# Kernel tuning notes

Measured on AMD Instinct MI355X. Metric: run time of the kernel, lower is better.

The kernel has to match this reference:

```python
import jax, jax.numpy as jnp
import numpy as np

GROUP_SIZE = 128
EQN = "btd,kdf->btkf"  # x:[B,T,D] @ w:[K,D,F] -> [B,T,K,F]


def setup_inputs() -> dict:
    key = jax.random.key(0)
    k1, k2, k3, k4 = jax.random.split(key, 4)
    B, T, D = 4, 2048, 4096
    K, F = 2, 8192
    G = D // GROUP_SIZE  # 32 quantization groups along D
    x = jax.random.normal(k1, (B, T, D), dtype=jnp.float32)
    qweight = jax.random.randint(k2, (K, D, F), 0, 16, dtype=jnp.int32)  # uint4 values
    qzeros = jax.random.randint(k3, (K, G, F), 0, 16, dtype=jnp.int32)   # uint4 zero points
    scales = jax.random.uniform(k4, (K, G, F), dtype=jnp.float32) * 0.02
    return {"x": x, "qweight": qweight, "qzeros": qzeros, "scales": scales}


def dequantize(imatrix, scales, zeros, group_size, axis_to_repeat):
    rs = jnp.repeat(scales, group_size, axis=axis_to_repeat)
    rz = jnp.repeat(zeros, group_size, axis=axis_to_repeat)
    return (imatrix.astype(rs.dtype) - rz.astype(rs.dtype)) * rs


def reference(x, qweight, qzeros, scales):
    # dequantize int4 weights along axis 1 (hidden/contraction dim), then einsum
    w = dequantize(qweight, scales, qzeros, GROUP_SIZE, axis_to_repeat=1)  # [K,D,F] fp32
    w = w.astype(x.dtype)
    return jnp.einsum(EQN, x, w)  # [B,T,K,F]
```

## Files before the change

kernel.cpp:

```cpp
#include <hip/hip_runtime.h>
#include <hip/hip_bf16.h>
#include <stdint.h>


typedef __attribute__((ext_vector_type(8))) short bf16x8;
typedef __attribute__((ext_vector_type(16))) float f32x16;
typedef __attribute__((ext_vector_type(4))) float f32x4;

static constexpr int Dd = 4096, Ff = 8192;
static constexpr int M = 8192, NTOT = 16384;
static constexpr int NKT = Dd / 64;
static constexpr int NMB = M / 256;
static constexpr int NNB = NTOT / 256;

__device__ __forceinline__ short f2bf(float f) {
    __hip_bfloat16 h = __float2bfloat16(f);
    return *reinterpret_cast<short*>(&h);
}

__device__ __forceinline__ int frag_off(int r, int cb) {
    const int rb = r >> 5, ks = cb >> 1, kh = cb & 1;
    return ((rb * 4 + ks) << 10) + (((r & 31) + 32 * kh) << 4);
}

__global__ __launch_bounds__(256) void xcvt(const float* __restrict__ x,
                                            char* __restrict__ Xw) {
    const int bid = blockIdx.x;
    const int h = bid >> 6, kt = bid & 63;
    const int t = threadIdx.x;
    const int r = t >> 1, seg = t & 1;
    const float* src = x + ((size_t)(h * 128 + r)) * Dd + kt * 64 + seg * 32;
    char* panel = Xw + ((size_t)bid << 14);
    #pragma unroll
    for (int jj = 0; jj < 4; ++jj) {
        float4 v0 = *reinterpret_cast<const float4*>(src + jj * 8);
        float4 v1 = *reinterpret_cast<const float4*>(src + jj * 8 + 4);
        union { short s[8]; bf16x8 v; } u;
        u.s[0] = f2bf(v0.x); u.s[1] = f2bf(v0.y); u.s[2] = f2bf(v0.z); u.s[3] = f2bf(v0.w);
        u.s[4] = f2bf(v1.x); u.s[5] = f2bf(v1.y); u.s[6] = f2bf(v1.z); u.s[7] = f2bf(v1.w);
        const int cb = seg * 4 + jj;
        *reinterpret_cast<bf16x8*>(panel + frag_off(r, cb)) = u.v;
    }
}

__global__ __launch_bounds__(256) void wdq(const int* __restrict__ qw,
                                           const int* __restrict__ qz,
                                           const float* __restrict__ sc,
                                           char* __restrict__ Ww) {
    const int bid = blockIdx.x;
    const int fh = bid >> 6, kt = bid & 63;
    const int t = threadIdx.x;
    const int r = t & 127, dh = t >> 7;
    const int n = fh * 128 + r;
    const int k = n >> 13, f = n & 8191;
    const int g = kt >> 1;
    const int   zv = qz[((size_t)k * 32 + g) * Ff + f];
    const float sv = sc[((size_t)k * 32 + g) * Ff + f];
    const int* qp = qw + ((size_t)(k * Dd + kt * 64 + dh * 32)) * Ff + f;
    char* panel = Ww + ((size_t)bid << 14);
    #pragma unroll
    for (int jj = 0; jj < 4; ++jj) {
        union { short s[8]; bf16x8 v; } u;
        #pragma unroll
        for (int e = 0; e < 8; ++e) {
            int q = qp[(size_t)(jj * 8 + e) * Ff];
            u.s[e] = f2bf((float)(q - zv) * sv);
        }
        const int cb = dh * 4 + jj;
        *reinterpret_cast<bf16x8*>(panel + frag_off(r, cb)) = u.v;
    }
}

#define APAN(HALF, KT) (Xw + (((size_t)(bm2 + (HALF)) * 64 + (KT)) << 14))
#define BPAN(HALF, KT) (Ww + (((size_t)(bn2 + (HALF)) * 64 + (KT)) << 14))

#define STAGE(GP, LP) do {                                                         \
    const char* _g = (GP) + woff16;                                                \
    char* _l = (LP) + woffu;                                                       \
    __builtin_amdgcn_global_load_lds(                                              \
        (const __attribute__((address_space(1))) void*)(_g),                       \
        (__attribute__((address_space(3))) void*)(_l), 16, 0, 0);                  \
    __builtin_amdgcn_global_load_lds(                                              \
        (const __attribute__((address_space(1))) void*)(_g + 8192),                \
        (__attribute__((address_space(3))) void*)(_l + 8192), 16, 0, 0);           \
} while (0)

#define PHASE(LA, LB, H, KS2, LOADB, STG, WAITQ) do {                              \
    if (LOADB) {                                                                   \
        _Pragma("unroll")                                                          \
        for (int nf = 0; nf < 2; ++nf)                                             \
            _Pragma("unroll")                                                      \
            for (int kq = 0; kq < 2; ++kq)                                         \
                bb[nf * 2 + kq] = *reinterpret_cast<const bf16x8*>(                \
                    (LB) + bbase + ((nf * 4 + (KS2) + kq) << 10) + lane16);        \
    }                                                                              \
    _Pragma("unroll")                                                              \
    for (int mf = 0; mf < 2; ++mf)                                                 \
        _Pragma("unroll")                                                          \
        for (int kq = 0; kq < 2; ++kq)                                             \
            af[mf * 2 + kq] = *reinterpret_cast<const bf16x8*>(                    \
                (LA) + abase + (((((H) * 2 + mf) * 4) + (KS2) + kq) << 10) + lane16); \
    STG;                                                                           \
    __builtin_amdgcn_sched_barrier(0);                                             \
    __builtin_amdgcn_s_barrier();                                                  \
    asm volatile("s_waitcnt lgkmcnt(0)" ::: "memory");                             \
    __builtin_amdgcn_sched_barrier(0);                                             \
    __builtin_amdgcn_s_setprio(1);                                                 \
    _Pragma("unroll")                                                              \
    for (int kq = 0; kq < 2; ++kq)                                                 \
        _Pragma("unroll")                                                          \
        for (int mf = 0; mf < 2; ++mf)                                             \
            _Pragma("unroll")                                                      \
            for (int nf = 0; nf < 2; ++nf)                                         \
                acc[((H) * 2 + mf) * 2 + nf] = __builtin_amdgcn_mfma_f32_32x32x16_bf16( \
                    af[mf * 2 + kq], bb[nf * 2 + kq],                              \
                    acc[((H) * 2 + mf) * 2 + nf], 0, 0, 0);                        \
    __builtin_amdgcn_s_setprio(0);                                                 \
    WAITQ;                                                                         \
    __builtin_amdgcn_sched_barrier(0);                                             \
    __builtin_amdgcn_s_barrier();                                                  \
} while (0)

__global__ __launch_bounds__(512, 2) void gemm256(const char* __restrict__ Xw,
                                                  const char* __restrict__ Ww,
                                                  float* __restrict__ out) {
    __shared__ char lds[131072];
    char* lA0 = lds;
    char* lB0 = lds + 32768;
    char* lA1 = lds + 65536;
    char* lB1 = lds + 98304;

    const int t = threadIdx.x;
    const int wave = t >> 6, lane = t & 63;
    const int wm = wave >> 2, wn = wave & 3;
    const int l31 = lane & 31;
    const int lane16 = lane << 4;

    const int xcd = blockIdx.x & 7;
    const int c   = blockIdx.x >> 3;
    const int bn  = xcd * 8 + (c >> 5);
    const int bm  = c & 31;
    const int bm2 = bm * 2, bn2 = bn * 2;

    const int woff16 = wave * 1024 + lane16;
    const int woffu  = wave * 1024;
    const int abase = wm * 16384;
    const int bbase = (wn >> 1) * 16384 + (wn & 1) * 8192;

    bf16x8 af[4], bb[4];
    f32x16 acc[8] = {};

    STAGE(APAN(0, 0), lA0);
    STAGE(APAN(1, 0), lA0 + 16384);
    STAGE(BPAN(0, 0), lB0);
    STAGE(BPAN(1, 0), lB0 + 16384);
    STAGE(BPAN(0, 1), lB1);
    asm volatile("s_waitcnt vmcnt(2)" ::: "memory");
    __builtin_amdgcn_sched_barrier(0);
    __builtin_amdgcn_s_barrier();

    for (int i = 0; i < 32; ++i) {
        const int kt0 = 2 * i;
        const bool nl = (i < 31);
        PHASE(lA0, lB0, 0, 0, 1, { STAGE(BPAN(1, kt0 + 1), lB1 + 16384); }, );
        PHASE(lA0, lB0, 1, 0, 0, { STAGE(APAN(0, kt0 + 1), lA1); }, );
        PHASE(lA0, lB0, 0, 2, 1, { STAGE(APAN(1, kt0 + 1), lA1 + 16384); }, );
        PHASE(lA0, lB0, 1, 2, 0, { if (nl) STAGE(BPAN(0, kt0 + 2), lB0); },
              { if (nl) asm volatile("s_waitcnt vmcnt(2)" ::: "memory");
                else    asm volatile("s_waitcnt vmcnt(0)" ::: "memory"); });
        PHASE(lA1, lB1, 0, 0, 1, { if (nl) STAGE(BPAN(1, kt0 + 2), lB0 + 16384); }, );
        PHASE(lA1, lB1, 1, 0, 0, { if (nl) STAGE(APAN(0, kt0 + 2), lA0); }, );
        PHASE(lA1, lB1, 0, 2, 1, { if (nl) STAGE(APAN(1, kt0 + 2), lA0 + 16384); }, );
        PHASE(lA1, lB1, 1, 2, 0, { if (nl) STAGE(BPAN(0, kt0 + 3), lB1); },
              { if (nl) asm volatile("s_waitcnt vmcnt(2)" ::: "memory");
                else    asm volatile("s_waitcnt vmcnt(0)" ::: "memory"); });
    }

    const int rbase = bm * 256 + wm * 128 + (lane >> 5) * 4;
    const int cbase = bn * 256 + wn * 64 + l31;
    #pragma unroll
    for (int mf = 0; mf < 4; ++mf)
        #pragma unroll
        for (int nf = 0; nf < 2; ++nf)
            #pragma unroll
            for (int reg = 0; reg < 16; ++reg) {
                const int row = rbase + mf * 32 + (reg & 3) + 8 * (reg >> 2);
                out[(size_t)row * NTOT + cbase + nf * 32] = acc[mf * 2 + nf][reg];
            }
}

#define LDP 72
__global__ __launch_bounds__(256) void int4_gemm(
    const float* __restrict__ x, const int* __restrict__ qw,
    const int* __restrict__ qz, const float* __restrict__ sc,
    float* __restrict__ out)
{
    __shared__ short As[128][LDP];
    __shared__ short Bs[128][LDP];
    const int t = threadIdx.x;
    int gid = (blockIdx.x & 7) * 1024 + (blockIdx.x >> 3);
    const int bm = gid & 63;
    const int bnq = gid >> 6;
    const int kse = bnq >> 6;
    const int f0  = (bnq & 63) * 128;
    const int m0  = bm * 128;
    const int wave = t >> 6, lane = t & 63;
    const int wm = wave >> 1, wn = wave & 1;
    const int l15 = lane & 15, lhi = lane >> 4;
    const int am = t >> 4, ad = (t & 15) * 4;
    const int bf = t & 127, bd = (t >> 7) * 4;
    const int*   qwk = qw + (size_t)kse * Dd * Ff;
    const int*   qzk = qz + (size_t)kse * 32 * Ff;
    const float* sck = sc + (size_t)kse * 32 * Ff;
    f32x4 acc[4][4] = {};
    for (int d0 = 0; d0 < Dd; d0 += 64) {
        __syncthreads();
        #pragma unroll
        for (int p = 0; p < 8; ++p) {
            int m = p * 16 + am;
            const float4 v = *reinterpret_cast<const float4*>(
                &x[(size_t)(m0 + m) * Dd + d0 + ad]);
            short4 wv;
            wv.x = f2bf(v.x); wv.y = f2bf(v.y); wv.z = f2bf(v.z); wv.w = f2bf(v.w);
            *reinterpret_cast<short4*>(&As[m][ad]) = wv;
        }
        {
            const int g = d0 >> 7;
            const int   zv = qzk[g * Ff + f0 + bf];
            const float sv = sck[g * Ff + f0 + bf];
            #pragma unroll
            for (int p = 0; p < 8; ++p) {
                int dl = p * 8 + bd;
                const int* qp = qwk + (size_t)(d0 + dl) * Ff + f0 + bf;
                short4 wv;
                wv.x = f2bf((float)(qp[0]      - zv) * sv);
                wv.y = f2bf((float)(qp[Ff]     - zv) * sv);
                wv.z = f2bf((float)(qp[2 * Ff] - zv) * sv);
                wv.w = f2bf((float)(qp[3 * Ff] - zv) * sv);
                *reinterpret_cast<short4*>(&Bs[bf][dl]) = wv;
            }
        }
        __syncthreads();
        #pragma unroll
        for (int kk = 0; kk < 64; kk += 32) {
            bf16x8 a2[4], b2[4];
            #pragma unroll
            for (int i = 0; i < 4; ++i)
                a2[i] = *reinterpret_cast<const bf16x8*>(&As[wm * 64 + i * 16 + l15][kk + lhi * 8]);
            #pragma unroll
            for (int i = 0; i < 4; ++i)
                b2[i] = *reinterpret_cast<const bf16x8*>(&Bs[wn * 64 + i * 16 + l15][kk + lhi * 8]);
            #pragma unroll
            for (int mi = 0; mi < 4; ++mi)
                #pragma unroll
                for (int ni = 0; ni < 4; ++ni)
                    acc[mi][ni] = __builtin_amdgcn_mfma_f32_16x16x32_bf16(
                        a2[mi], b2[ni], acc[mi][ni], 0, 0, 0);
        }
    }
    const int crow0 = m0 + wm * 64 + lhi * 4;
    const int ccol0 = bnq * 128 + wn * 64 + l15;
    #pragma unroll
    for (int mi = 0; mi < 4; ++mi)
        #pragma unroll
        for (int ni = 0; ni < 4; ++ni)
            #pragma unroll
            for (int r = 0; r < 4; ++r)
                out[(size_t)(crow0 + mi * 16 + r) * NTOT + ccol0 + ni * 16] =
                    acc[mi][ni][r];
}

extern "C" void kernel_launch(void* const* d_in, const int* in_sizes, int n_in,
                              void* d_out, int out_size, void* d_ws, size_t ws_size,
                              hipStream_t stream) {
    const float* x  = (const float*)d_in[0];
    const int*   qw = (const int*)d_in[1];
    const int*   qz = (const int*)d_in[2];
    const float* sc = (const float*)d_in[3];
    float*       out = (float*)d_out;

    const size_t xw_bytes = (size_t)(M / 128) * NKT * 16384;
    const size_t ww_bytes = (size_t)(NTOT / 128) * NKT * 16384;

    if (ws_size >= xw_bytes + ww_bytes) {
        char* Xw = (char*)d_ws;
        char* Ww = Xw + xw_bytes;
        hipLaunchKernelGGL(xcvt, dim3((M / 128) * NKT), dim3(256), 0, stream, x, Xw);
        hipLaunchKernelGGL(wdq, dim3((NTOT / 128) * NKT), dim3(256), 0, stream,
                           qw, qz, sc, Ww);
        hipLaunchKernelGGL(gemm256, dim3(NMB * NNB), dim3(512), 0, stream,
                           Xw, Ww, out);
    } else {
        hipLaunchKernelGGL(int4_gemm, dim3(8192), dim3(256), 0, stream,
                           x, qw, qz, sc, out);
    }
}
```

Before: 1.146 ms.

## Double-buffer LDS fragment registers to overlap reads with MFMA in gemm256

Restructures the main loop so LDS fragment reads for the next MFMA group go into a second register set (afX/afY, bbX/bbY) and are issued before the current MFMA group, rather than being waited on with lgkmcnt(0) right before each compute phase. The goal is to hide LDS read latency behind matrix-core work. In exchange it adds more s_barriers per iteration and more vector registers, which could hurt occupancy at 2 blocks per CU. Without an explicit lgkmcnt wait, correctness depends on the compiler inserting waits before the MFMAs consume the fragments.

```diff
diff --git a/kernel.cpp b/kernel.cpp
--- a/kernel.cpp
+++ b/kernel.cpp
@@ -85,26 +85,28 @@
         (__attribute__((address_space(3))) void*)(_l + 8192), 16, 0, 0);           \
 } while (0)
 
-#define PHASE(LA, LB, H, KS2, LOADB, STG, WAITQ) do {                              \
-    if (LOADB) {                                                                   \
-        _Pragma("unroll")                                                          \
-        for (int nf = 0; nf < 2; ++nf)                                             \
-            _Pragma("unroll")                                                      \
-            for (int kq = 0; kq < 2; ++kq)                                         \
-                bb[nf * 2 + kq] = *reinterpret_cast<const bf16x8*>(                \
-                    (LB) + bbase + ((nf * 4 + (KS2) + kq) << 10) + lane16);        \
-    }                                                                              \
+#define SB0() __builtin_amdgcn_sched_barrier(0)
+#define BARW() do { SB0(); __builtin_amdgcn_s_barrier(); SB0(); } while (0)
+
+#define RDA4(DST, LA, H, KS2) do {                                                 \
     _Pragma("unroll")                                                              \
     for (int mf = 0; mf < 2; ++mf)                                                 \
         _Pragma("unroll")                                                          \
         for (int kq = 0; kq < 2; ++kq)                                             \
-            af[mf * 2 + kq] = *reinterpret_cast<const bf16x8*>(                    \
+            DST[mf * 2 + kq] = *reinterpret_cast<const bf16x8*>(                   \
                 (LA) + abase + (((((H) * 2 + mf) * 4) + (KS2) + kq) << 10) + lane16); \
-    STG;                                                                           \
-    __builtin_amdgcn_sched_barrier(0);                                             \
-    __builtin_amdgcn_s_barrier();                                                  \
-    asm volatile("s_waitcnt lgkmcnt(0)" ::: "memory");                             \
-    __builtin_amdgcn_sched_barrier(0);                                             \
+} while (0)
+
+#define RDB4(DST, LB, KS2) do {                                                    \
+    _Pragma("unroll")                                                              \
+    for (int nf = 0; nf < 2; ++nf)                                                 \
+        _Pragma("unroll")                                                          \
+        for (int kq = 0; kq < 2; ++kq)                                             \
+            DST[nf * 2 + kq] = *reinterpret_cast<const bf16x8*>(                   \
+                (LB) + bbase + ((nf * 4 + (KS2) + kq) << 10) + lane16);            \
+} while (0)
+
+#define MM(H, AF, BB) do {                                                         \
     __builtin_amdgcn_s_setprio(1);                                                 \
     _Pragma("unroll")                                                              \
     for (int kq = 0; kq < 2; ++kq)                                                 \
@@ -113,12 +115,9 @@
             _Pragma("unroll")                                                      \
             for (int nf = 0; nf < 2; ++nf)                                         \
                 acc[((H) * 2 + mf) * 2 + nf] = __builtin_amdgcn_mfma_f32_32x32x16_bf16( \
-                    af[mf * 2 + kq], bb[nf * 2 + kq],                              \
+                    AF[mf * 2 + kq], BB[nf * 2 + kq],                              \
                     acc[((H) * 2 + mf) * 2 + nf], 0, 0, 0);                        \
     __builtin_amdgcn_s_setprio(0);                                                 \
-    WAITQ;                                                                         \
-    __builtin_amdgcn_sched_barrier(0);                                             \
-    __builtin_amdgcn_s_barrier();                                                  \
 } while (0)
 
 __global__ __launch_bounds__(512, 2) void gemm256(const char* __restrict__ Xw,
@@ -147,7 +146,7 @@
     const int abase = wm * 16384;
     const int bbase = (wn >> 1) * 16384 + (wn & 1) * 8192;
 
-    bf16x8 af[4], bb[4];
+    bf16x8 afX[4], afY[4], bbX[4], bbY[4];
     f32x16 acc[8] = {};
 
     STAGE(APAN(0, 0), lA0);
@@ -156,24 +155,63 @@
     STAGE(BPAN(1, 0), lB0 + 16384);
     STAGE(BPAN(0, 1), lB1);
     asm volatile("s_waitcnt vmcnt(2)" ::: "memory");
-    __builtin_amdgcn_sched_barrier(0);
-    __builtin_amdgcn_s_barrier();
+    BARW();
 
     for (int i = 0; i < 32; ++i) {
         const int kt0 = 2 * i;
         const bool nl = (i < 31);
-        PHASE(lA0, lB0, 0, 0, 1, { STAGE(BPAN(1, kt0 + 1), lB1 + 16384); }, );
-        PHASE(lA0, lB0, 1, 0, 0, { STAGE(APAN(0, kt0 + 1), lA1); }, );
-        PHASE(lA0, lB0, 0, 2, 1, { STAGE(APAN(1, kt0 + 1), lA1 + 16384); }, );
-        PHASE(lA0, lB0, 1, 2, 0, { if (nl) STAGE(BPAN(0, kt0 + 2), lB0); },
-              { if (nl) asm volatile("s_waitcnt vmcnt(2)" ::: "memory");
-                else    asm volatile("s_waitcnt vmcnt(0)" ::: "memory"); });
-        PHASE(lA1, lB1, 0, 0, 1, { if (nl) STAGE(BPAN(1, kt0 + 2), lB0 + 16384); }, );
-        PHASE(lA1, lB1, 1, 0, 0, { if (nl) STAGE(APAN(0, kt0 + 2), lA0); }, );
-        PHASE(lA1, lB1, 0, 2, 1, { if (nl) STAGE(APAN(1, kt0 + 2), lA0 + 16384); }, );
-        PHASE(lA1, lB1, 1, 2, 0, { if (nl) STAGE(BPAN(0, kt0 + 3), lB1); },
-              { if (nl) asm volatile("s_waitcnt vmcnt(2)" ::: "memory");
-                else    asm volatile("s_waitcnt vmcnt(0)" ::: "memory"); });
+        STAGE(BPAN(1, kt0 + 1), lB1 + 16384);
+        BARW();
+        RDB4(bbX, lB0, 0); RDA4(afX, lA0, 0, 0);
+        RDA4(afY, lA0, 1, 0);
+        SB0();
+        MM(0, afX, bbX);
+        BARW();
+        STAGE(APAN(0, kt0 + 1), lA1);
+        BARW();
+        RDB4(bbY, lB0, 2); RDA4(afX, lA0, 0, 2);
+        SB0();
+        MM(1, afY, bbX);
+        BARW();
+        STAGE(APAN(1, kt0 + 1), lA1 + 16384);
+        BARW();
+        RDA4(afY, lA0, 1, 2);
+        SB0();
+        MM(0, afX, bbY);
+        BARW();
+        if (nl) STAGE(BPAN(0, kt0 + 2), lB0);
+        BARW();
+        SB0();
+        MM(1, afY, bbY);
+        if (nl) asm volatile("s_waitcnt vmcnt(2)" ::: "memory");
+        else    asm volatile("s_waitcnt vmcnt(0)" ::: "memory");
+        BARW();
+        if (nl) STAGE(BPAN(1, kt0 + 2), lB0 + 16384);
+        BARW();
+        RDB4(bbX, lB1, 0); RDA4(afX, lA1, 0, 0);
+        RDA4(afY, lA1, 1, 0);
+        SB0();
+        MM(0, afX, bbX);
+        BARW();
+        if (nl) STAGE(APAN(0, kt0 + 2), lA0);
+        BARW();
+        RDB4(bbY, lB1, 2); RDA4(afX, lA1, 0, 2);
+        SB0();
+        MM(1, afY, bbX);
+        BARW();
+        if (nl) STAGE(APAN(1, kt0 + 2), lA0 + 16384);
+        BARW();
+        RDA4(afY, lA1, 1, 2);
+        SB0();
+        MM(0, afX, bbY);
+        BARW();
+        if (nl) STAGE(BPAN(0, kt0 + 3), lB1);
+        BARW();
+        SB0();
+        MM(1, afY, bbY);
+        if (nl) asm volatile("s_waitcnt vmcnt(2)" ::: "memory");
+        else    asm volatile("s_waitcnt vmcnt(0)" ::: "memory");
+        BARW();
     }
 
     const int rbase = bm * 256 + wm * 128 + (lane >> 5) * 4;
```

Result: no change. 1.151 ms (+0.4%).

## Restructure GEMM pipeline to four-stage 32-wide K tiles with per-tile barriers

Applied to the files above, without the earlier changes.

Pre-packed panels go from 64-wide to 32-wide K slices, and the main GEMM loop changes from an 8-phase double buffer with two barriers per phase to a 4-deep LDS ring. Each body stages the tile two steps ahead, does all 16 MFMAs for the tile, then waits and syncs once. The output stores become nontemporal. This is meant to cut barrier and wait overhead and keep more loads in flight, at the cost of a changed panel layout and less interleaving of LDS reads with MFMAs inside a tile.

```diff
diff --git a/kernel.cpp b/kernel.cpp
--- a/kernel.cpp
+++ b/kernel.cpp
@@ -9,7 +9,7 @@
 
 static constexpr int Dd = 4096, Ff = 8192;
 static constexpr int M = 8192, NTOT = 16384;
-static constexpr int NKT = Dd / 64;
+static constexpr int NKT2 = Dd / 32;
 static constexpr int NMB = M / 256;
 static constexpr int NNB = NTOT / 256;
 
@@ -18,28 +18,28 @@
     return *reinterpret_cast<short*>(&h);
 }
 
-__device__ __forceinline__ int frag_off(int r, int cb) {
+__device__ __forceinline__ int frag_off32(int r, int cb) {
     const int rb = r >> 5, ks = cb >> 1, kh = cb & 1;
-    return ((rb * 4 + ks) << 10) + (((r & 31) + 32 * kh) << 4);
+    return ((rb * 2 + ks) << 10) + (((r & 31) + 32 * kh) << 4);
 }
 
 __global__ __launch_bounds__(256) void xcvt(const float* __restrict__ x,
                                             char* __restrict__ Xw) {
     const int bid = blockIdx.x;
-    const int h = bid >> 6, kt = bid & 63;
+    const int h = bid >> 7, kt2 = bid & 127;
     const int t = threadIdx.x;
     const int r = t >> 1, seg = t & 1;
-    const float* src = x + ((size_t)(h * 128 + r)) * Dd + kt * 64 + seg * 32;
-    char* panel = Xw + ((size_t)bid << 14);
-    #pragma unroll
-    for (int jj = 0; jj < 4; ++jj) {
+    const float* src = x + ((size_t)(h * 128 + r)) * Dd + kt2 * 32 + seg * 16;
+    char* panel = Xw + ((size_t)bid << 13);
+    #pragma unroll
+    for (int jj = 0; jj < 2; ++jj) {
         float4 v0 = *reinterpret_cast<const float4*>(src + jj * 8);
         float4 v1 = *reinterpret_cast<const float4*>(src + jj * 8 + 4);
         union { short s[8]; bf16x8 v; } u;
         u.s[0] = f2bf(v0.x); u.s[1] = f2bf(v0.y); u.s[2] = f2bf(v0.z); u.s[3] = f2bf(v0.w);
         u.s[4] = f2bf(v1.x); u.s[5] = f2bf(v1.y); u.s[6] = f2bf(v1.z); u.s[7] = f2bf(v1.w);
-        const int cb = seg * 4 + jj;
-        *reinterpret_cast<bf16x8*>(panel + frag_off(r, cb)) = u.v;
+        const int cb = seg * 2 + jj;
+        *reinterpret_cast<bf16x8*>(panel + frag_off32(r, cb)) = u.v;
     }
 }
 
@@ -48,87 +48,84 @@
                                            const float* __restrict__ sc,
                                            char* __restrict__ Ww) {
     const int bid = blockIdx.x;
-    const int fh = bid >> 6, kt = bid & 63;
+    const int fh = bid >> 7, kt2 = bid & 127;
     const int t = threadIdx.x;
     const int r = t & 127, dh = t >> 7;
     const int n = fh * 128 + r;
     const int k = n >> 13, f = n & 8191;
-    const int g = kt >> 1;
+    const int g = kt2 >> 2;
     const int   zv = qz[((size_t)k * 32 + g) * Ff + f];
     const float sv = sc[((size_t)k * 32 + g) * Ff + f];
-    const int* qp = qw + ((size_t)(k * Dd + kt * 64 + dh * 32)) * Ff + f;
-    char* panel = Ww + ((size_t)bid << 14);
-    #pragma unroll
-    for (int jj = 0; jj < 4; ++jj) {
+    const int* qp = qw + ((size_t)(k * Dd + kt2 * 32 + dh * 16)) * Ff + f;
+    char* panel = Ww + ((size_t)bid << 13);
+    #pragma unroll
+    for (int jj = 0; jj < 2; ++jj) {
         union { short s[8]; bf16x8 v; } u;
         #pragma unroll
         for (int e = 0; e < 8; ++e) {
             int q = qp[(size_t)(jj * 8 + e) * Ff];
             u.s[e] = f2bf((float)(q - zv) * sv);
         }
-        const int cb = dh * 4 + jj;
-        *reinterpret_cast<bf16x8*>(panel + frag_off(r, cb)) = u.v;
-    }
-}
-
-#define APAN(HALF, KT) (Xw + (((size_t)(bm2 + (HALF)) * 64 + (KT)) << 14))
-#define BPAN(HALF, KT) (Ww + (((size_t)(bn2 + (HALF)) * 64 + (KT)) << 14))
-
-#define STAGE(GP, LP) do {                                                         \
-    const char* _g = (GP) + woff16;                                                \
-    char* _l = (LP) + woffu;                                                       \
+        const int cb = dh * 2 + jj;
+        *reinterpret_cast<bf16x8*>(panel + frag_off32(r, cb)) = u.v;
+    }
+}
+
+#define APAN32(H, KT2) (Xw + (((size_t)(H) * 128 + (KT2)) << 13))
+#define BPAN32(H, KT2) (Ww + (((size_t)(H) * 128 + (KT2)) << 13))
+
+#define GLL(GP, LP)                                                                \
     __builtin_amdgcn_global_load_lds(                                              \
-        (const __attribute__((address_space(1))) void*)(_g),                       \
-        (__attribute__((address_space(3))) void*)(_l), 16, 0, 0);                  \
-    __builtin_amdgcn_global_load_lds(                                              \
-        (const __attribute__((address_space(1))) void*)(_g + 8192),                \
-        (__attribute__((address_space(3))) void*)(_l + 8192), 16, 0, 0);           \
+        (const __attribute__((address_space(1))) void*)(GP),                       \
+        (__attribute__((address_space(3))) void*)(LP), 16, 0, 0)
+
+#define STAGE_TILE(KT2, BUF) do {                                                  \
+    GLL(APAN32(bm2,     (KT2)) + woff16, (BUF) +     0 + woffu);                   \
+    GLL(APAN32(bm2 + 1, (KT2)) + woff16, (BUF) +  8192 + woffu);                   \
+    GLL(BPAN32(bn2,     (KT2)) + woff16, (BUF) + 16384 + woffu);                   \
+    GLL(BPAN32(bn2 + 1, (KT2)) + woff16, (BUF) + 24576 + woffu);                   \
 } while (0)
 
-#define PHASE(LA, LB, H, KS2, LOADB, STG, WAITQ) do {                              \
-    if (LOADB) {                                                                   \
+#define SB0() __builtin_amdgcn_sched_barrier(0)
+
+#define BODY(KT2, BUFR, DOST, BUFS) do {                                           \
+    if (DOST) STAGE_TILE((KT2) + 2, BUFS);                                         \
+    bf16x8 a[8], b[4];                                                             \
+    _Pragma("unroll")                                                              \
+    for (int mb = 0; mb < 4; ++mb)                                                 \
         _Pragma("unroll")                                                          \
-        for (int nf = 0; nf < 2; ++nf)                                             \
-            _Pragma("unroll")                                                      \
-            for (int kq = 0; kq < 2; ++kq)                                         \
-                bb[nf * 2 + kq] = *reinterpret_cast<const bf16x8*>(                \
-                    (LB) + bbase + ((nf * 4 + (KS2) + kq) << 10) + lane16);        \
-    }                                                                              \
+        for (int ks = 0; ks < 2; ++ks)                                             \
+            a[mb * 2 + ks] = *reinterpret_cast<const bf16x8*>(                     \
+                (BUFR) + aoff + (mb * 2 + ks) * 1024);                             \
     _Pragma("unroll")                                                              \
-    for (int mf = 0; mf < 2; ++mf)                                                 \
+    for (int nf = 0; nf < 2; ++nf)                                                 \
         _Pragma("unroll")                                                          \
-        for (int kq = 0; kq < 2; ++kq)                                             \
-            af[mf * 2 + kq] = *reinterpret_cast<const bf16x8*>(                    \
-                (LA) + abase + (((((H) * 2 + mf) * 4) + (KS2) + kq) << 10) + lane16); \
-    STG;                                                                           \
-    __builtin_amdgcn_sched_barrier(0);                                             \
-    __builtin_amdgcn_s_barrier();                                                  \
-    asm volatile("s_waitcnt lgkmcnt(0)" ::: "memory");                             \
-    __builtin_amdgcn_sched_barrier(0);                                             \
-    __builtin_amdgcn_s_setprio(1);                                                 \
+        for (int ks = 0; ks < 2; ++ks)                                             \
+            b[nf * 2 + ks] = *reinterpret_cast<const bf16x8*>(                     \
+                (BUFR) + boff + nf * 2048 + ks * 1024);                            \
     _Pragma("unroll")                                                              \
-    for (int kq = 0; kq < 2; ++kq)                                                 \
+    for (int ks = 0; ks < 2; ++ks)                                                 \
         _Pragma("unroll")                                                          \
-        for (int mf = 0; mf < 2; ++mf)                                             \
+        for (int mb = 0; mb < 4; ++mb)                                             \
             _Pragma("unroll")                                                      \
             for (int nf = 0; nf < 2; ++nf)                                         \
-                acc[((H) * 2 + mf) * 2 + nf] = __builtin_amdgcn_mfma_f32_32x32x16_bf16( \
-                    af[mf * 2 + kq], bb[nf * 2 + kq],                              \
-                    acc[((H) * 2 + mf) * 2 + nf], 0, 0, 0);                        \
-    __builtin_amdgcn_s_setprio(0);                                                 \
-    WAITQ;                                                                         \
-    __builtin_amdgcn_sched_barrier(0);                                             \
+                acc[mb * 2 + nf] = __builtin_amdgcn_mfma_f32_32x32x16_bf16(        \
+                    a[mb * 2 + ks], b[nf * 2 + ks], acc[mb * 2 + nf], 0, 0, 0);    \
+    if (DOST) asm volatile("s_waitcnt vmcnt(4)" ::: "memory");                     \
+    else      asm volatile("s_waitcnt vmcnt(0)" ::: "memory");                     \
+    SB0();                                                                         \
     __builtin_amdgcn_s_barrier();                                                  \
+    SB0();                                                                         \
 } while (0)
 
 __global__ __launch_bounds__(512, 2) void gemm256(const char* __restrict__ Xw,
                                                   const char* __restrict__ Ww,
                                                   float* __restrict__ out) {
     __shared__ char lds[131072];
-    char* lA0 = lds;
-    char* lB0 = lds + 32768;
-    char* lA1 = lds + 65536;
-    char* lB1 = lds + 98304;
+    char* const L0 = lds;
+    char* const L1 = lds + 32768;
+    char* const L2 = lds + 65536;
+    char* const L3 = lds + 98304;
 
     const int t = threadIdx.x;
     const int wave = t >> 6, lane = t & 63;
@@ -144,48 +141,39 @@
 
     const int woff16 = wave * 1024 + lane16;
     const int woffu  = wave * 1024;
-    const int abase = wm * 16384;
-    const int bbase = (wn >> 1) * 16384 + (wn & 1) * 8192;
-
-    bf16x8 af[4], bb[4];
+    const int aoff = wm * 8192 + lane16;
+    const int boff = 16384 + (wn >> 1) * 8192 + (wn & 1) * 4096 + lane16;
+
     f32x16 acc[8] = {};
 
-    STAGE(APAN(0, 0), lA0);
-    STAGE(APAN(1, 0), lA0 + 16384);
-    STAGE(BPAN(0, 0), lB0);
-    STAGE(BPAN(1, 0), lB0 + 16384);
-    STAGE(BPAN(0, 1), lB1);
-    asm volatile("s_waitcnt vmcnt(2)" ::: "memory");
-    __builtin_amdgcn_sched_barrier(0);
+    STAGE_TILE(0, L0);
+    STAGE_TILE(1, L1);
+    asm volatile("s_waitcnt vmcnt(4)" ::: "memory");
+    SB0();
     __builtin_amdgcn_s_barrier();
+    SB0();
 
     for (int i = 0; i < 32; ++i) {
-        const int kt0 = 2 * i;
+        const int T = i * 4;
         const bool nl = (i < 31);
-        PHASE(lA0, lB0, 0, 0, 1, { STAGE(BPAN(1, kt0 + 1), lB1 + 16384); }, );
-        PHASE(lA0, lB0, 1, 0, 0, { STAGE(APAN(0, kt0 + 1), lA1); }, );
-        PHASE(lA0, lB0, 0, 2, 1, { STAGE(APAN(1, kt0 + 1), lA1 + 16384); }, );
-        PHASE(lA0, lB0, 1, 2, 0, { if (nl) STAGE(BPAN(0, kt0 + 2), lB0); },
-              { if (nl) asm volatile("s_waitcnt vmcnt(2)" ::: "memory");
-                else    asm volatile("s_waitcnt vmcnt(0)" ::: "memory"); });
-        PHASE(lA1, lB1, 0, 0, 1, { if (nl) STAGE(BPAN(1, kt0 + 2), lB0 + 16384); }, );
-        PHASE(lA1, lB1, 1, 0, 0, { if (nl) STAGE(APAN(0, kt0 + 2), lA0); }, );
-        PHASE(lA1, lB1, 0, 2, 1, { if (nl) STAGE(APAN(1, kt0 + 2), lA0 + 16384); }, );
-        PHASE(lA1, lB1, 1, 2, 0, { if (nl) STAGE(BPAN(0, kt0 + 3), lB1); },
-              { if (nl) asm volatile("s_waitcnt vmcnt(2)" ::: "memory");
-                else    asm volatile("s_waitcnt vmcnt(0)" ::: "memory"); });
+        BODY(T + 0, L0, true, L2);
+        BODY(T + 1, L1, true, L3);
+        BODY(T + 2, L2, nl,   L0);
+        BODY(T + 3, L3, nl,   L1);
     }
 
     const int rbase = bm * 256 + wm * 128 + (lane >> 5) * 4;
     const int cbase = bn * 256 + wn * 64 + l31;
     #pragma unroll
-    for (int mf = 0; mf < 4; ++mf)
+    for (int mb = 0; mb < 4; ++mb)
         #pragma unroll
         for (int nf = 0; nf < 2; ++nf)
             #pragma unroll
             for (int reg = 0; reg < 16; ++reg) {
-                const int row = rbase + mf * 32 + (reg & 3) + 8 * (reg >> 2);
-                out[(size_t)row * NTOT + cbase + nf * 32] = acc[mf * 2 + nf][reg];
+                const int row = rbase + mb * 32 + (reg & 3) + 8 * (reg >> 2);
+                __builtin_nontemporal_store(
+                    acc[mb * 2 + nf][reg],
+                    &out[(size_t)row * NTOT + cbase + nf * 32]);
             }
 }
 
@@ -279,14 +267,14 @@
     const float* sc = (const float*)d_in[3];
     float*       out = (float*)d_out;
 
-    const size_t xw_bytes = (size_t)(M / 128) * NKT * 16384;
-    const size_t ww_bytes = (size_t)(NTOT / 128) * NKT * 16384;
+    const size_t xw_bytes = (size_t)(M / 128) * NKT2 * 8192;
+    const size_t ww_bytes = (size_t)(NTOT / 128) * NKT2 * 8192;
 
     if (ws_size >= xw_bytes + ww_bytes) {
         char* Xw = (char*)d_ws;
         char* Ww = Xw + xw_bytes;
-        hipLaunchKernelGGL(xcvt, dim3((M / 128) * NKT), dim3(256), 0, stream, x, Xw);
-        hipLaunchKernelGGL(wdq, dim3((NTOT / 128) * NKT), dim3(256), 0, stream,
+        hipLaunchKernelGGL(xcvt, dim3((M / 128) * NKT2), dim3(256), 0, stream, x, Xw);
+        hipLaunchKernelGGL(wdq, dim3((NTOT / 128) * NKT2), dim3(256), 0, stream,
                            qw, qz, sc, Ww);
         hipLaunchKernelGGL(gemm256, dim3(NMB * NNB), dim3(512), 0, stream,
                            Xw, Ww, out);
```

Measured after the change: 1.155 ms. No clear change (+0.8%).
